# Optimization experiments

Measured on AMD Instinct MI355X. Metric: run time of the kernel, lower is better.

Reference implementation:

```python
import jax, jax.numpy as jnp
import numpy as np


def setup_inputs() -> dict:
    key = jax.random.key(0)
    k1, k2 = jax.random.split(key)
    d, T, n = 256, 8192, 64
    # scale down so exp(ht^T D^T D hj) stays in range, as typical trained D would
    H = jax.random.normal(k1, (d, T), dtype=jnp.float32) * 0.1
    D = jax.random.normal(k2, (n, d), dtype=jnp.float32) * 0.1
    l2 = jnp.ones((), dtype=jnp.float32)
    return {"H": H, "D": D, "l2": l2}


def reference(H, D, l2):
    # H: [d, T], D: [n, d]
    DH = D @ H                                   # [n, T] = D @ H_T.T
    # S[t, j] = h_t^T (D^T D) h_j  == (DH)^T (DH)
    S = jnp.einsum('nt,nj->tj', DH, DH)          # [T, T]
    # beta_j = exp(-0.5 * ||D h_j||^2); row t: attn[t,:] = beta * exp(S[t,:]) / sum
    log_beta = -0.5 * jnp.sum(DH * DH, axis=0)   # [T]
    attn_map = jax.nn.softmax(S + log_beta[None, :], axis=1)  # [T, T]
    Z = l2 * (H @ attn_map)                      # [d, T]
    return Z
```

## Files before the change

kernel.cpp:

```cpp
#include <hip/hip_runtime.h>

#define T_DIM 8192
#define D_DIM 256
#define N_DIM 64
#define LOG2E 1.44269504f

typedef __bf16 bf16x8 __attribute__((ext_vector_type(8)));
typedef __bf16 bf16x4 __attribute__((ext_vector_type(4)));
typedef float f32x16 __attribute__((ext_vector_type(16)));

__device__ __forceinline__ f32x16 zero16() {
  f32x16 v;
#pragma unroll
  for (int i = 0; i < 16; ++i) v[i] = 0.f;
  return v;
}


__global__ __launch_bounds__(256) void k_dh(const float* __restrict__ H,
                                            const float* __restrict__ Dm,
                                            __bf16* __restrict__ DHf,
                                            float* __restrict__ lbe,
                                            float* __restrict__ rowsum) {
  __shared__ __bf16 HlThi[64 * 264];
  __shared__ __bf16 HlTlo[64 * 264];
  __shared__ __bf16 DHs[64 * 72];
  const int tid = threadIdx.x;
  const int t0 = blockIdx.x * 64;
  const int lane = tid & 63;
  const int wave = tid >> 6;
  const int h = lane >> 5;
  const int l31 = lane & 31;
  const float4* H4 = (const float4*)H;
#pragma unroll
  for (int r = 0; r < 16; ++r) {
    int idx = r * 256 + tid;
    int d = idx >> 4, tc = idx & 15;
    float4 v = H4[(size_t)d * (T_DIM / 4) + (t0 >> 2) + tc];
    float vv[4] = {v.x, v.y, v.z, v.w};
#pragma unroll
    for (int i = 0; i < 4; ++i) {
      __bf16 hi = (__bf16)vv[i];
      float lo = vv[i] - (float)hi;
      HlThi[(tc * 4 + i) * 264 + d] = hi;
      HlTlo[(tc * 4 + i) * 264 + d] = (__bf16)lo;
    }
  }
  __syncthreads();
  const int tt = wave & 1, nh = wave >> 1;
  const int m = tt * 32 + l31;
  const int n = nh * 32 + l31;
  f32x16 c = zero16();
  for (int kk = 0; kk < 16; ++kk) {
    bf16x8 ahi = *(const bf16x8*)&HlThi[m * 264 + kk * 16 + h * 8];
    bf16x8 alo = *(const bf16x8*)&HlTlo[m * 264 + kk * 16 + h * 8];
    const float4* dp = (const float4*)(Dm + (size_t)n * 256 + kk * 16 + h * 8);
    float4 b0 = dp[0], b1 = dp[1];
    float bv[8] = {b0.x, b0.y, b0.z, b0.w, b1.x, b1.y, b1.z, b1.w};
    bf16x8 bhi, blo;
#pragma unroll
    for (int i = 0; i < 8; ++i) {
      __bf16 hi = (__bf16)bv[i];
      bhi[i] = hi;
      blo[i] = (__bf16)(bv[i] - (float)hi);
    }
    c = __builtin_amdgcn_mfma_f32_32x32x16_bf16(ahi, bhi, c, 0, 0, 0);
    c = __builtin_amdgcn_mfma_f32_32x32x16_bf16(ahi, blo, c, 0, 0, 0);
    c = __builtin_amdgcn_mfma_f32_32x32x16_bf16(alo, bhi, c, 0, 0, 0);
  }
#pragma unroll
  for (int r = 0; r < 16; ++r) {
    int row = tt * 32 + (r & 3) + 8 * (r >> 2) + 4 * h;
    DHs[row * 72 + n] = (__bf16)c[r];
  }
  __syncthreads();
#pragma unroll
  for (int r = 0; r < 2; ++r) {
    int idx = r * 256 + tid;
    int g = idx >> 8, cc = (idx >> 5) & 7, l = idx & 31;
    bf16x8 w = *(const bf16x8*)&DHs[(g * 32 + l) * 72 + cc * 8];
    *(bf16x8*)(DHf + (size_t)(blockIdx.x * 2 + g) * 2048 + cc * 256 + l * 8) = w;
  }
  if (tid < 64) {
    float s = 0.f;
#pragma unroll
    for (int q = 0; q < 8; ++q) {
      bf16x8 w = *(const bf16x8*)&DHs[tid * 72 + q * 8];
#pragma unroll
      for (int i = 0; i < 8; ++i) { float f = (float)w[i]; s += f * f; }
    }
    lbe[t0 + tid] = -0.5f * s * LOG2E;
    rowsum[t0 + tid] = 0.f;
  }
}

__global__ __launch_bounds__(512, 4) void k_rowsum(const __bf16* __restrict__ DHf,
                                                   const float* __restrict__ lbe,
                                                   float* __restrict__ rowsum) {
  __shared__ float red2[256][33];
  const int tid = threadIdx.x;
  const int lane = tid & 63;
  const int wave = tid >> 6;
  const int h = lane >> 5;
  const int l31 = lane & 31;
  const int t0 = (int)(blockIdx.x >> 4) * 256;
  const int jbase = (int)(blockIdx.x & 15) * 512;
  const size_t Gt = (size_t)(t0 >> 5) + wave;
  const size_t Gj0 = (size_t)(jbase >> 5);
  bf16x8 aR[4];
#pragma unroll
  for (int kk = 0; kk < 4; ++kk)
    aR[kk] = *(const bf16x8*)(DHf + Gt * 2048 + kk * 512 + lane * 8);
  float racc[16];
#pragma unroll
  for (int r = 0; r < 16; ++r) racc[r] = 0.f;
  bf16x8 b0[4], b1[4];
#pragma unroll
  for (int kk = 0; kk < 4; ++kk) {
    b0[kk] = *(const bf16x8*)(DHf + Gj0 * 2048 + kk * 512 + lane * 8);
    b1[kk] = *(const bf16x8*)(DHf + (Gj0 + 1) * 2048 + kk * 512 + lane * 8);
  }
#pragma unroll
  for (int jj = 0; jj < 8; ++jj) {
    {
      const float lbv = lbe[jbase + (jj * 2) * 32 + l31];
      f32x16 s0 = zero16(), s1 = zero16();
      s0 = __builtin_amdgcn_mfma_f32_32x32x16_bf16(aR[0], b0[0], s0, 0, 0, 0);
      s1 = __builtin_amdgcn_mfma_f32_32x32x16_bf16(aR[1], b0[1], s1, 0, 0, 0);
      s0 = __builtin_amdgcn_mfma_f32_32x32x16_bf16(aR[2], b0[2], s0, 0, 0, 0);
      s1 = __builtin_amdgcn_mfma_f32_32x32x16_bf16(aR[3], b0[3], s1, 0, 0, 0);
      if (jj < 7) {
        const size_t Gj = Gj0 + jj * 2 + 2;
#pragma unroll
        for (int kk = 0; kk < 4; ++kk)
          b0[kk] = *(const bf16x8*)(DHf + Gj * 2048 + kk * 512 + lane * 8);
      }
#pragma unroll
      for (int r = 0; r < 16; ++r)
        racc[r] += __builtin_amdgcn_exp2f(
            __builtin_fmaf(s0[r] + s1[r], LOG2E, lbv));
    }
    {
      const float lbv = lbe[jbase + (jj * 2 + 1) * 32 + l31];
      f32x16 s0 = zero16(), s1 = zero16();
      s0 = __builtin_amdgcn_mfma_f32_32x32x16_bf16(aR[0], b1[0], s0, 0, 0, 0);
      s1 = __builtin_amdgcn_mfma_f32_32x32x16_bf16(aR[1], b1[1], s1, 0, 0, 0);
      s0 = __builtin_amdgcn_mfma_f32_32x32x16_bf16(aR[2], b1[2], s0, 0, 0, 0);
      s1 = __builtin_amdgcn_mfma_f32_32x32x16_bf16(aR[3], b1[3], s1, 0, 0, 0);
      if (jj < 7) {
        const size_t Gj = Gj0 + jj * 2 + 3;
#pragma unroll
        for (int kk = 0; kk < 4; ++kk)
          b1[kk] = *(const bf16x8*)(DHf + Gj * 2048 + kk * 512 + lane * 8);
      }
#pragma unroll
      for (int r = 0; r < 16; ++r)
        racc[r] += __builtin_amdgcn_exp2f(
            __builtin_fmaf(s0[r] + s1[r], LOG2E, lbv));
    }
  }
#pragma unroll
  for (int r = 0; r < 16; ++r) {
    int tl = wave * 32 + (r & 3) + 8 * (r >> 2) + 4 * h;
    red2[tl][l31] = racc[r];
  }
  __syncthreads();
  if (tid < 256) {
    float s = 0.f;
#pragma unroll 8
    for (int c = 0; c < 32; ++c) s += red2[tid][c];
    atomicAdd(&rowsum[t0 + tid], s);
  }
}

__global__ __launch_bounds__(256) void k_scaleH(const float* __restrict__ H,
                                                const float* __restrict__ rowsum,
                                                __bf16* __restrict__ Hbf_sw) {
  __shared__ float rinvL[64];
  const int tid = threadIdx.x;
  const int bx = blockIdx.x;
  const int tblk = bx >> 1, dh = bx & 1;
  const int t0 = tblk * 64;
  if (tid < 64) rinvL[tid] = 1.0f / rowsum[t0 + tid];
  __syncthreads();
#pragma unroll
  for (int itr = 0; itr < 4; ++itr) {
    int idx = itr * 256 + tid;
    int dl = idx >> 3, tbp = idx & 7;
    int d = dh * 128 + dl;
    int swz = (d ^ (d >> 3)) & 7;
    int tloc = (tbp ^ swz) << 3;
    const float4* hp = (const float4*)(H + (size_t)d * T_DIM + t0 + tloc);
    float4 v0 = hp[0], v1 = hp[1];
    float4 r0 = *(const float4*)&rinvL[tloc];
    float4 r1 = *(const float4*)&rinvL[tloc + 4];
    bf16x8 w;
    w[0] = (__bf16)(v0.x * r0.x); w[1] = (__bf16)(v0.y * r0.y);
    w[2] = (__bf16)(v0.z * r0.z); w[3] = (__bf16)(v0.w * r0.w);
    w[4] = (__bf16)(v1.x * r1.x); w[5] = (__bf16)(v1.y * r1.y);
    w[6] = (__bf16)(v1.z * r1.z); w[7] = (__bf16)(v1.w * r1.w);
    *(bf16x8*)(Hbf_sw + (size_t)tblk * 16384 + (size_t)d * 64 + tbp * 8) = w;
  }
}

__global__ __launch_bounds__(512, 4) void k_z(const __bf16* __restrict__ Hbf_sw,
                                              const __bf16* __restrict__ DHf,
                                              const float* __restrict__ lbe,
                                              float* __restrict__ Zp) {
  __shared__ __bf16 Hs[2][128 * 64];
  __shared__ __bf16 Pt[2][128 * 64];
  const int tid = threadIdx.x;
  const int lane = tid & 63;
  const int wave = tid >> 6;
  const int h = lane >> 5;
  const int l31 = lane & 31;
  const int bx = blockIdx.x;
  const int ts = bx & 3;
  const int dh = (bx >> 2) & 1;
  const int j0 = (bx >> 3) * 128;
  const int s_tt = wave & 1, s_jg = wave >> 1;
  const int dq = wave & 1, jv = wave >> 1;
  bf16x8 bS[4];
  float lbv;
  {
    const size_t Gj = (size_t)(j0 >> 5) + s_jg;
#pragma unroll
    for (int kk = 0; kk < 4; ++kk)
      bS[kk] = *(const bf16x8*)(DHf + Gj * 2048 + kk * 512 + lane * 8);
    lbv = lbe[j0 + s_jg * 32 + l31];
  }
  f32x16 acc[2];
#pragma unroll
  for (int u = 0; u < 2; ++u) acc[u] = zero16();

#define DMA_HS(buf_, it_)                                                       \
  {                                                                             \
    const __bf16* gsrc =                                                        \
        Hbf_sw + (size_t)(ts * 32 + (it_)) * 16384 + (size_t)dh * 8192;         \
    _Pragma("unroll") for (int r = 0; r < 2; ++r) {                             \
      int chunk = wave * 2 + r;                                                 \
      __builtin_amdgcn_global_load_lds(                                         \
          (const __attribute__((address_space(1))) unsigned int*)(gsrc +        \
              chunk * 512 + lane * 8),                                          \
          (__attribute__((address_space(3))) unsigned int*)(&Hs[buf_][0] +      \
              chunk * 512),                                                     \
          16, 0, 0);                                                            \
    }                                                                           \
  }

#define LOAD_AR(reg_, n_)                                                       \
  {                                                                             \
    const size_t Gt_ = (size_t)(ts * 64 + (n_)*2 + s_tt);                       \
    _Pragma("unroll") for (int kk = 0; kk < 4; ++kk)                            \
        (reg_)[kk] = *(const bf16x8*)(DHf + Gt_ * 2048 + kk * 512 + lane * 8);  \
  }

#define S_PHASE(p_, reg_)                                                       \
  {                                                                             \
    f32x16 s = zero16();                                                        \
    s = __builtin_amdgcn_mfma_f32_32x32x16_bf16((reg_)[0], bS[0], s, 0, 0, 0);  \
    s = __builtin_amdgcn_mfma_f32_32x32x16_bf16((reg_)[1], bS[1], s, 0, 0, 0);  \
    s = __builtin_amdgcn_mfma_f32_32x32x16_bf16((reg_)[2], bS[2], s, 0, 0, 0);  \
    s = __builtin_amdgcn_mfma_f32_32x32x16_bf16((reg_)[3], bS[3], s, 0, 0, 0);  \
    const int jl = s_jg * 32 + l31;                                             \
    const int sj = (jl ^ (jl >> 3)) & 7;                                        \
    _Pragma("unroll") for (int g = 0; g < 4; ++g) {                             \
      const int tl = s_tt * 32 + g * 8 + 4 * h;                                 \
      bf16x4 pv;                                                                \
      pv[0] = (__bf16)__builtin_amdgcn_exp2f(                                   \
          __builtin_fmaf(s[g * 4 + 0], LOG2E, lbv));                            \
      pv[1] = (__bf16)__builtin_amdgcn_exp2f(                                   \
          __builtin_fmaf(s[g * 4 + 1], LOG2E, lbv));                            \
      pv[2] = (__bf16)__builtin_amdgcn_exp2f(                                   \
          __builtin_fmaf(s[g * 4 + 2], LOG2E, lbv));                            \
      pv[3] = (__bf16)__builtin_amdgcn_exp2f(                                   \
          __builtin_fmaf(s[g * 4 + 3], LOG2E, lbv));                            \
      const int cchunk = tl >> 3;                                               \
      *(bf16x4*)&Pt[p_][jl * 64 + ((cchunk ^ sj) << 3) + 4 * h] = pv;           \
    }                                                                           \
  }

#define Z_PHASE(p_)                                                             \
  {                                                                             \
    __builtin_amdgcn_s_setprio(1);                                              \
    _Pragma("unroll") for (int kk = 0; kk < 4; ++kk) {                          \
      const int c = kk * 2 + h;                                                 \
      bf16x8 af[2], bw;                                                         \
      _Pragma("unroll") for (int u = 0; u < 2; ++u) {                           \
        int dl = dq * 64 + u * 32 + l31;                                        \
        af[u] =                                                                 \
            *(const bf16x8*)&Hs[p_][dl * 64 + ((c ^ ((dl ^ (dl >> 3)) & 7)) << 3)]; \
      }                                                                         \
      {                                                                         \
        int j = jv * 32 + l31;                                                  \
        bw = *(const bf16x8*)&Pt[p_][j * 64 + ((c ^ ((j ^ (j >> 3)) & 7)) << 3)]; \
      }                                                                         \
      _Pragma("unroll") for (int u = 0; u < 2; ++u)                             \
          acc[u] = __builtin_amdgcn_mfma_f32_32x32x16_bf16(af[u], bw, acc[u],   \
                                                           0, 0, 0);            \
    }                                                                           \
    __builtin_amdgcn_s_setprio(0);                                              \
  }

  bf16x8 aR[4], aRn[4];
  LOAD_AR(aR, 0);
  DMA_HS(0, 0);
  S_PHASE(0, aR);
  LOAD_AR(aRn, 1);
  __syncthreads();

  for (int ii = 0; ii < 16; ++ii) {
    const int it0 = ii * 2;
    DMA_HS(1, it0 + 1);
    if (it0 < 30) LOAD_AR(aR, it0 + 2);
    S_PHASE(1, aRn);
    Z_PHASE(0);
    __syncthreads();
    if (it0 + 1 < 31) {
      DMA_HS(0, it0 + 2);
      S_PHASE(0, aR);
    }
    if (it0 + 1 < 30) LOAD_AR(aRn, it0 + 3);
    Z_PHASE(1);
    __syncthreads();
  }
#undef Z_PHASE
#undef S_PHASE
#undef LOAD_AR
#undef DMA_HS
  float* zp = Zp + (size_t)ts * (256 * (size_t)T_DIM);
#pragma unroll
  for (int u = 0; u < 2; ++u)
#pragma unroll
    for (int r = 0; r < 16; ++r) {
      int d = dh * 128 + dq * 64 + u * 32 + (r & 3) + 8 * (r >> 2) + 4 * h;
      int j = j0 + jv * 32 + l31;
      zp[(size_t)d * T_DIM + j] = acc[u][r];
    }
}

__global__ __launch_bounds__(256) void k_zred(const float* __restrict__ Zp,
                                              const float* __restrict__ l2p,
                                              float* __restrict__ Z) {
  const int i = blockIdx.x * 256 + threadIdx.x;
  const float l2v = l2p[0];
  const float4* zp4 = (const float4*)Zp;
  float4 a = zp4[i];
#pragma unroll
  for (int s = 1; s < 4; ++s) {
    float4 b = zp4[(size_t)s * 524288 + i];
    a.x += b.x; a.y += b.y; a.z += b.z; a.w += b.w;
  }
  float4 o = {a.x * l2v, a.y * l2v, a.z * l2v, a.w * l2v};
  ((float4*)Z)[i] = o;
}

extern "C" void kernel_launch(void* const* d_in, const int* in_sizes, int n_in,
                              void* d_out, int out_size, void* d_ws,
                              size_t ws_size, hipStream_t stream) {
  (void)in_sizes; (void)n_in; (void)out_size; (void)ws_size;
  const float* H = (const float*)d_in[0];
  const float* Dm = (const float*)d_in[1];
  const float* l2 = (const float*)d_in[2];
  float* Z = (float*)d_out;
  char* ws = (char*)d_ws;
  __bf16* DHf = (__bf16*)ws;
  float* lbe = (float*)(ws + 1048576);
  float* rowsum = (float*)(ws + 1048576 + 32768);
  __bf16* Hbf_sw = (__bf16*)(ws + 1114112);
  float* Zp = (float*)(ws + 5308416);

  k_dh<<<128, 256, 0, stream>>>(H, Dm, DHf, lbe, rowsum);
  k_rowsum<<<512, 512, 0, stream>>>(DHf, lbe, rowsum);
  k_scaleH<<<256, 256, 0, stream>>>(H, rowsum, Hbf_sw);
  k_z<<<512, 512, 0, stream>>>(Hbf_sw, DHf, lbe, Zp);
  k_zred<<<2048, 256, 0, stream>>>(Zp, l2, Z);
}
```

Baseline: 148.4 us.

## Fuse H row-scaling into attention kernel and split DH kernel over K

Removes the separate k_scaleH pass. k_z now loads fp32 H directly from global memory into registers, scales it by the reciprocal row sums cached in LDS, and writes bf16 into the swizzled LDS buffer, with register staging in place of async global_load_lds. Separately, k_dh uses 32-token blocks with the K dimension split across wave pairs and reduced through LDS, which doubles the grid to 256 blocks. The intent is to save a kernel launch and the bf16 round trip through global memory. In exchange, k_z loads twice as many bytes of H, uses more registers and 8KB more LDS, and adds an extra sync at the prologue.

```diff
diff --git a/kernel.cpp b/kernel.cpp
--- a/kernel.cpp
+++ b/kernel.cpp
@@ -22,20 +22,21 @@
                                             __bf16* __restrict__ DHf,
                                             float* __restrict__ lbe,
                                             float* __restrict__ rowsum) {
-  __shared__ __bf16 HlThi[64 * 264];
-  __shared__ __bf16 HlTlo[64 * 264];
-  __shared__ __bf16 DHs[64 * 72];
+  __shared__ __bf16 HlThi[32 * 264];
+  __shared__ __bf16 HlTlo[32 * 264];
+  __shared__ __bf16 DHs[32 * 72];
+  __shared__ float redf[2][32][33];
   const int tid = threadIdx.x;
-  const int t0 = blockIdx.x * 64;
+  const int t0 = blockIdx.x * 32;
   const int lane = tid & 63;
   const int wave = tid >> 6;
   const int h = lane >> 5;
   const int l31 = lane & 31;
   const float4* H4 = (const float4*)H;
 #pragma unroll
-  for (int r = 0; r < 16; ++r) {
+  for (int r = 0; r < 8; ++r) {
     int idx = r * 256 + tid;
-    int d = idx >> 4, tc = idx & 15;
+    int d = idx >> 3, tc = idx & 7;
     float4 v = H4[(size_t)d * (T_DIM / 4) + (t0 >> 2) + tc];
     float vv[4] = {v.x, v.y, v.z, v.w};
 #pragma unroll
@@ -47,11 +48,14 @@
     }
   }
   __syncthreads();
-  const int tt = wave & 1, nh = wave >> 1;
-  const int m = tt * 32 + l31;
+  const int nh = wave & 1;
+  const int kh = wave >> 1;
+  const int m = l31;
   const int n = nh * 32 + l31;
   f32x16 c = zero16();
-  for (int kk = 0; kk < 16; ++kk) {
+#pragma unroll
+  for (int kq = 0; kq < 8; ++kq) {
+    const int kk = kh * 8 + kq;
     bf16x8 ahi = *(const bf16x8*)&HlThi[m * 264 + kk * 16 + h * 8];
     bf16x8 alo = *(const bf16x8*)&HlTlo[m * 264 + kk * 16 + h * 8];
     const float4* dp = (const float4*)(Dm + (size_t)n * 256 + kk * 16 + h * 8);
@@ -68,20 +72,28 @@
     c = __builtin_amdgcn_mfma_f32_32x32x16_bf16(ahi, blo, c, 0, 0, 0);
     c = __builtin_amdgcn_mfma_f32_32x32x16_bf16(alo, bhi, c, 0, 0, 0);
   }
-#pragma unroll
-  for (int r = 0; r < 16; ++r) {
-    int row = tt * 32 + (r & 3) + 8 * (r >> 2) + 4 * h;
-    DHs[row * 72 + n] = (__bf16)c[r];
-  }
-  __syncthreads();
-#pragma unroll
-  for (int r = 0; r < 2; ++r) {
-    int idx = r * 256 + tid;
-    int g = idx >> 8, cc = (idx >> 5) & 7, l = idx & 31;
-    bf16x8 w = *(const bf16x8*)&DHs[(g * 32 + l) * 72 + cc * 8];
-    *(bf16x8*)(DHf + (size_t)(blockIdx.x * 2 + g) * 2048 + cc * 256 + l * 8) = w;
-  }
-  if (tid < 64) {
+  if (kh == 1) {
+#pragma unroll
+    for (int r = 0; r < 16; ++r) {
+      int row = (r & 3) + 8 * (r >> 2) + 4 * h;
+      redf[nh][row][l31] = c[r];
+    }
+  }
+  __syncthreads();
+  if (kh == 0) {
+#pragma unroll
+    for (int r = 0; r < 16; ++r) {
+      int row = (r & 3) + 8 * (r >> 2) + 4 * h;
+      DHs[row * 72 + n] = (__bf16)(c[r] + redf[nh][row][l31]);
+    }
+  }
+  __syncthreads();
+  {
+    int cc = tid >> 5, l = tid & 31;
+    bf16x8 w = *(const bf16x8*)&DHs[l * 72 + cc * 8];
+    *(bf16x8*)(DHf + (size_t)blockIdx.x * 2048 + cc * 256 + l * 8) = w;
+  }
+  if (tid < 32) {
     float s = 0.f;
 #pragma unroll
     for (int q = 0; q < 8; ++q) {
@@ -173,42 +185,14 @@
   }
 }
 
-__global__ __launch_bounds__(256) void k_scaleH(const float* __restrict__ H,
-                                                const float* __restrict__ rowsum,
-                                                __bf16* __restrict__ Hbf_sw) {
-  __shared__ float rinvL[64];
-  const int tid = threadIdx.x;
-  const int bx = blockIdx.x;
-  const int tblk = bx >> 1, dh = bx & 1;
-  const int t0 = tblk * 64;
-  if (tid < 64) rinvL[tid] = 1.0f / rowsum[t0 + tid];
-  __syncthreads();
-#pragma unroll
-  for (int itr = 0; itr < 4; ++itr) {
-    int idx = itr * 256 + tid;
-    int dl = idx >> 3, tbp = idx & 7;
-    int d = dh * 128 + dl;
-    int swz = (d ^ (d >> 3)) & 7;
-    int tloc = (tbp ^ swz) << 3;
-    const float4* hp = (const float4*)(H + (size_t)d * T_DIM + t0 + tloc);
-    float4 v0 = hp[0], v1 = hp[1];
-    float4 r0 = *(const float4*)&rinvL[tloc];
-    float4 r1 = *(const float4*)&rinvL[tloc + 4];
-    bf16x8 w;
-    w[0] = (__bf16)(v0.x * r0.x); w[1] = (__bf16)(v0.y * r0.y);
-    w[2] = (__bf16)(v0.z * r0.z); w[3] = (__bf16)(v0.w * r0.w);
-    w[4] = (__bf16)(v1.x * r1.x); w[5] = (__bf16)(v1.y * r1.y);
-    w[6] = (__bf16)(v1.z * r1.z); w[7] = (__bf16)(v1.w * r1.w);
-    *(bf16x8*)(Hbf_sw + (size_t)tblk * 16384 + (size_t)d * 64 + tbp * 8) = w;
-  }
-}
-
-__global__ __launch_bounds__(512, 4) void k_z(const __bf16* __restrict__ Hbf_sw,
+__global__ __launch_bounds__(512, 4) void k_z(const float* __restrict__ H,
                                               const __bf16* __restrict__ DHf,
                                               const float* __restrict__ lbe,
+                                              const float* __restrict__ rowsum,
                                               float* __restrict__ Zp) {
   __shared__ __bf16 Hs[2][128 * 64];
   __shared__ __bf16 Pt[2][128 * 64];
+  __shared__ float rinvL[2048];
   const int tid = threadIdx.x;
   const int lane = tid & 63;
   const int wave = tid >> 6;
@@ -220,6 +204,19 @@
   const int j0 = (bx >> 3) * 128;
   const int s_tt = wave & 1, s_jg = wave >> 1;
   const int dq = wave & 1, jv = wave >> 1;
+  const int dl0 = tid >> 3, tbp0 = tid & 7;
+  const int dl1 = (tid + 512) >> 3, tbp1 = tid & 7;
+  const int d0 = dh * 128 + dl0, d1 = dh * 128 + dl1;
+  const int tl0 = ((tbp0 ^ ((d0 ^ (d0 >> 3)) & 7)) << 3);
+  const int tl1 = ((tbp1 ^ ((d1 ^ (d1 >> 3)) & 7)) << 3);
+  const float* hrow0 = H + (size_t)d0 * T_DIM + ts * 2048;
+  const float* hrow1 = H + (size_t)d1 * T_DIM + ts * 2048;
+  const int lds0 = dl0 * 64 + tbp0 * 8, lds1 = dl1 * 64 + tbp1 * 8;
+#pragma unroll
+  for (int k2 = 0; k2 < 4; ++k2) {
+    int i = k2 * 512 + tid;
+    rinvL[i] = 1.0f / rowsum[ts * 2048 + i];
+  }
   bf16x8 bS[4];
   float lbv;
   {
@@ -232,20 +229,36 @@
   f32x16 acc[2];
 #pragma unroll
   for (int u = 0; u < 2; ++u) acc[u] = zero16();
-
-#define DMA_HS(buf_, it_)                                                       \
-  {                                                                             \
-    const __bf16* gsrc =                                                        \
-        Hbf_sw + (size_t)(ts * 32 + (it_)) * 16384 + (size_t)dh * 8192;         \
-    _Pragma("unroll") for (int r = 0; r < 2; ++r) {                             \
-      int chunk = wave * 2 + r;                                                 \
-      __builtin_amdgcn_global_load_lds(                                         \
-          (const __attribute__((address_space(1))) unsigned int*)(gsrc +        \
-              chunk * 512 + lane * 8),                                          \
-          (__attribute__((address_space(3))) unsigned int*)(&Hs[buf_][0] +      \
-              chunk * 512),                                                     \
-          16, 0, 0);                                                            \
-    }                                                                           \
+  float4 hA0, hA1, hB0, hB1;
+
+#define STAGE_ISSUE(it_)                                                        \
+  {                                                                             \
+    const int tb_ = (it_)*64;                                                   \
+    hA0 = *(const float4*)(hrow0 + tb_ + tl0);                                  \
+    hA1 = *(const float4*)(hrow0 + tb_ + tl0 + 4);                              \
+    hB0 = *(const float4*)(hrow1 + tb_ + tl1);                                  \
+    hB1 = *(const float4*)(hrow1 + tb_ + tl1 + 4);                              \
+  }
+
+#define STAGE_WRITE(buf_, it_)                                                  \
+  {                                                                             \
+    const int tb_ = (it_)*64;                                                   \
+    float4 r0 = *(const float4*)&rinvL[tb_ + tl0];                              \
+    float4 r1 = *(const float4*)&rinvL[tb_ + tl0 + 4];                          \
+    bf16x8 w;                                                                   \
+    w[0] = (__bf16)(hA0.x * r0.x); w[1] = (__bf16)(hA0.y * r0.y);               \
+    w[2] = (__bf16)(hA0.z * r0.z); w[3] = (__bf16)(hA0.w * r0.w);               \
+    w[4] = (__bf16)(hA1.x * r1.x); w[5] = (__bf16)(hA1.y * r1.y);               \
+    w[6] = (__bf16)(hA1.z * r1.z); w[7] = (__bf16)(hA1.w * r1.w);               \
+    *(bf16x8*)&Hs[buf_][lds0] = w;                                              \
+    float4 r2 = *(const float4*)&rinvL[tb_ + tl1];                              \
+    float4 r3 = *(const float4*)&rinvL[tb_ + tl1 + 4];                          \
+    bf16x8 w2;                                                                  \
+    w2[0] = (__bf16)(hB0.x * r2.x); w2[1] = (__bf16)(hB0.y * r2.y);             \
+    w2[2] = (__bf16)(hB0.z * r2.z); w2[3] = (__bf16)(hB0.w * r2.w);             \
+    w2[4] = (__bf16)(hB1.x * r3.x); w2[5] = (__bf16)(hB1.y * r3.y);             \
+    w2[6] = (__bf16)(hB1.z * r3.z); w2[7] = (__bf16)(hB1.w * r3.w);             \
+    *(bf16x8*)&Hs[buf_][lds1] = w2;                                             \
   }
 
 #define LOAD_AR(reg_, n_)                                                       \
@@ -304,30 +317,35 @@
 
   bf16x8 aR[4], aRn[4];
   LOAD_AR(aR, 0);
-  DMA_HS(0, 0);
+  STAGE_ISSUE(0);
+  __syncthreads();
   S_PHASE(0, aR);
   LOAD_AR(aRn, 1);
+  STAGE_WRITE(0, 0);
   __syncthreads();
 
   for (int ii = 0; ii < 16; ++ii) {
     const int it0 = ii * 2;
-    DMA_HS(1, it0 + 1);
+    STAGE_ISSUE(it0 + 1);
     if (it0 < 30) LOAD_AR(aR, it0 + 2);
     S_PHASE(1, aRn);
     Z_PHASE(0);
+    STAGE_WRITE(1, it0 + 1);
     __syncthreads();
     if (it0 + 1 < 31) {
-      DMA_HS(0, it0 + 2);
+      STAGE_ISSUE(it0 + 2);
       S_PHASE(0, aR);
     }
     if (it0 + 1 < 30) LOAD_AR(aRn, it0 + 3);
     Z_PHASE(1);
+    if (it0 + 1 < 31) STAGE_WRITE(0, it0 + 2);
     __syncthreads();
   }
 #undef Z_PHASE
 #undef S_PHASE
 #undef LOAD_AR
-#undef DMA_HS
+#undef STAGE_WRITE
+#undef STAGE_ISSUE
   float* zp = Zp + (size_t)ts * (256 * (size_t)T_DIM);
 #pragma unroll
   for (int u = 0; u < 2; ++u)
@@ -367,12 +385,10 @@
   __bf16* DHf = (__bf16*)ws;
   float* lbe = (float*)(ws + 1048576);
   float* rowsum = (float*)(ws + 1048576 + 32768);
-  __bf16* Hbf_sw = (__bf16*)(ws + 1114112);
-  float* Zp = (float*)(ws + 5308416);
-
-  k_dh<<<128, 256, 0, stream>>>(H, Dm, DHf, lbe, rowsum);
+  float* Zp = (float*)(ws + 1114112);
+
+  k_dh<<<256, 256, 0, stream>>>(H, Dm, DHf, lbe, rowsum);
   k_rowsum<<<512, 512, 0, stream>>>(DHf, lbe, rowsum);
-  k_scaleH<<<256, 256, 0, stream>>>(H, rowsum, Hbf_sw);
-  k_z<<<512, 512, 0, stream>>>(Hbf_sw, DHf, lbe, Zp);
+  k_z<<<512, 512, 0, stream>>>(H, DHf, lbe, rowsum, Zp);
   k_zred<<<2048, 256, 0, stream>>>(Zp, l2, Z);
 }
```

Result: slower. 156.6 us (+5.5%).
